# Optimization experiments

Hardware: AMD Instinct MI355X
Metric: run time of the kernel (lower is better)

The kernel has to match this reference:

```python
import jax, jax.numpy as jnp
import numpy as np

N = 50000   # nodes
E = 1000000 # edges
D_IN = 64
D_OUT = 64
R = 16      # relations (num_rels == num_bases)


def setup_inputs() -> dict:
    key = jax.random.key(0)
    k1, k2, k3, k4, k5, k6, k7 = jax.random.split(key, 7)
    node_features = jax.random.normal(k1, (N, D_IN), dtype=jnp.float32)
    edge_src = jax.random.randint(k2, (E,), 0, N, dtype=jnp.int32)
    edge_dst = jax.random.randint(k3, (E,), 0, N, dtype=jnp.int32)
    edge_type = jax.random.randint(k4, (E,), 0, R, dtype=jnp.int32)
    edge_norm = jax.random.uniform(k5, (E,), dtype=jnp.float32)
    weight = jax.random.normal(k6, (R, D_IN, D_OUT), dtype=jnp.float32) * 0.1
    bias = jax.random.normal(k7, (D_OUT,), dtype=jnp.float32) * 0.1
    return {
        "node_features": node_features,
        "edge_src": edge_src,
        "edge_dst": edge_dst,
        "edge_type": edge_type,
        "edge_norm": edge_norm,
        "weight": weight,
        "bias": bias,
    }


def reference(node_features, edge_src, edge_dst, edge_type, edge_norm, weight, bias):
    # gather source features and per-edge relation weight matrices
    h_src = node_features[edge_src]              # [E, D_IN]
    w = weight[edge_type]                        # [E, D_IN, D_OUT]
    # per-edge bmm: [E,1,D_IN] @ [E,D_IN,D_OUT] -> [E,D_OUT]
    msg = jnp.einsum('ed,edo->eo', h_src, w)
    msg = msg * edge_norm[:, None]               # norm scaling
    # scatter-sum aggregation over destination nodes
    node_repr = jax.ops.segment_sum(msg, edge_dst, num_segments=N)  # [N, D_OUT]
    node_repr = node_repr + bias
    return jax.nn.relu(node_repr)
```

## Files before the change

kernel.cpp:

```cpp
#include <hip/hip_runtime.h>
#include <hip/hip_bf16.h>


#define NN 50000
#define EE 1000000
#define RR 16
#define NBLK 256
#define EPB 3907
#define BSH 6
#define NBUK 782
#define NS (NBUK * NBLK)
#define SCAP 2048

typedef __attribute__((ext_vector_type(8))) short short8;
typedef __attribute__((ext_vector_type(4))) float f32x4;

static __device__ inline unsigned short f2bf(float f) {
  union { __hip_bfloat16 h; unsigned short u; } cv;
  cv.h = __float2bfloat16(f);
  return cv.u;
}
static __device__ inline float bf2f(unsigned short u) {
  union { unsigned i; float f; } cv;
  cv.i = ((unsigned)u) << 16;
  return cv.f;
}

__global__ __launch_bounds__(256) void k_wt(const float* __restrict__ W,
                                            unsigned short* __restrict__ Wt) {
  __shared__ __align__(16) unsigned short Wl[64][72];
  const int r = blockIdx.x, tid = threadIdx.x;
  for (int i = tid; i < 4096; i += 256) Wl[i & 63][i >> 6] = f2bf(W[(r << 12) + i]);
  __syncthreads();
  const int o = tid >> 2, kc = (tid & 3) << 4;
  const short8 v0 = *reinterpret_cast<const short8*>(&Wl[o][kc]);
  const short8 v1 = *reinterpret_cast<const short8*>(&Wl[o][kc + 8]);
  unsigned short* dst = Wt + (r << 12) + (o << 6) + kc;
  *reinterpret_cast<short8*>(dst) = v0;
  *reinterpret_cast<short8*>(dst + 8) = v1;
}

__global__ __launch_bounds__(256) void k_gemm_hist(const float* __restrict__ nf,
                                                   const unsigned short* __restrict__ Wt,
                                                   const int* __restrict__ edst,
                                                   unsigned short* __restrict__ X,
                                                   int* __restrict__ cntT) {
  __shared__ __align__(16) char smem[4 * 64 * 72 * 2];
  const int bid = blockIdx.x, tid = threadIdx.x;
  if (bid < NBLK) {
    int* cnt = reinterpret_cast<int*>(smem);
    for (int i = tid; i < NBUK; i += 256) cnt[i] = 0;
    __syncthreads();
    const int e0 = bid * EPB, e1 = min(EE, e0 + EPB);
    for (int e = e0 + tid; e < e1; e += 256) atomicAdd(&cnt[edst[e] >> BSH], 1);
    __syncthreads();
    for (int i = tid; i < NBUK; i += 256) cntT[i * NBLK + bid] = cnt[i];
    return;
  }
  auto Wl = reinterpret_cast<unsigned short(*)[64][72]>(smem);
  const int g = bid - NBLK;
  const int bx = g >> 2, r0 = (g & 3) << 2;
  const int lane = tid & 63, wv = tid >> 6;
  const int lr = lane & 15, lg = lane >> 4;
  const int node = (bx << 6) + (wv << 4) + lr;
  #pragma unroll
  for (int rr = 0; rr < 4; ++rr) {
    const unsigned short* src = Wt + (((size_t)(r0 + rr)) << 12) + (tid << 4);
    const short8 v0 = *reinterpret_cast<const short8*>(src);
    const short8 v1 = *reinterpret_cast<const short8*>(src + 8);
    unsigned short* dst = &Wl[rr][tid >> 2][(tid & 3) << 4];
    *reinterpret_cast<short8*>(dst) = v0;
    *reinterpret_cast<short8*>(dst + 8) = v1;
  }
  short8 bf0, bf1;
  if (node < NN) {
    const float* ap = nf + (size_t)node * 64 + lg * 8;
    float4 v0 = *reinterpret_cast<const float4*>(ap);
    float4 v1 = *reinterpret_cast<const float4*>(ap + 4);
    float4 v2 = *reinterpret_cast<const float4*>(ap + 32);
    float4 v3 = *reinterpret_cast<const float4*>(ap + 36);
    bf0 = short8{(short)f2bf(v0.x), (short)f2bf(v0.y), (short)f2bf(v0.z), (short)f2bf(v0.w),
                 (short)f2bf(v1.x), (short)f2bf(v1.y), (short)f2bf(v1.z), (short)f2bf(v1.w)};
    bf1 = short8{(short)f2bf(v2.x), (short)f2bf(v2.y), (short)f2bf(v2.z), (short)f2bf(v2.w),
                 (short)f2bf(v3.x), (short)f2bf(v3.y), (short)f2bf(v3.z), (short)f2bf(v3.w)};
  } else {
    bf0 = short8{0, 0, 0, 0, 0, 0, 0, 0};
    bf1 = bf0;
  }
  __syncthreads();
  #pragma unroll
  for (int rr = 0; rr < 4; ++rr) {
    const int r = r0 + rr;
    short8 a[8];
    #pragma unroll
    for (int c = 0; c < 4; ++c) {
      a[2 * c] = *reinterpret_cast<const short8*>(&Wl[rr][(c << 4) + lr][lg << 3]);
      a[2 * c + 1] = *reinterpret_cast<const short8*>(&Wl[rr][(c << 4) + lr][32 + (lg << 3)]);
    }
    f32x4 acc[4];
    #pragma unroll
    for (int c = 0; c < 4; ++c) {
      acc[c] = f32x4{0.f, 0.f, 0.f, 0.f};
      acc[c] = __builtin_amdgcn_mfma_f32_16x16x32_bf16(a[2 * c], bf0, acc[c], 0, 0, 0);
      acc[c] = __builtin_amdgcn_mfma_f32_16x16x32_bf16(a[2 * c + 1], bf1, acc[c], 0, 0, 0);
    }
    if (node < NN) {
      #pragma unroll
      for (int c = 0; c < 4; ++c) {
        uint2 p;
        p.x = (unsigned)f2bf(acc[c][0]) | ((unsigned)f2bf(acc[c][1]) << 16);
        p.y = (unsigned)f2bf(acc[c][2]) | ((unsigned)f2bf(acc[c][3]) << 16);
        *reinterpret_cast<uint2*>(&X[((size_t)r * NN + node) * 64 + (c << 4) + (lg << 2)]) = p;
      }
    }
  }
}

__global__ __launch_bounds__(256) void k_scan_a(const int* __restrict__ cntT,
                                                int* __restrict__ offsT,
                                                int* __restrict__ bsum) {
  __shared__ int s[256];
  const int t = threadIdx.x;
  const int i = blockIdx.x * 256 + t;
  const int v = cntT[i];
  s[t] = v;
  __syncthreads();
  #pragma unroll
  for (int off = 1; off < 256; off <<= 1) {
    const int x = (t >= off) ? s[t - off] : 0;
    __syncthreads();
    s[t] += x;
    __syncthreads();
  }
  offsT[i] = s[t] - v;
  if (t == 255) bsum[blockIdx.x] = s[255];
}

__global__ __launch_bounds__(1024) void k_scan_b(const int* __restrict__ bsum,
                                                 int* __restrict__ bsum2) {
  __shared__ int s[1024];
  const int t = threadIdx.x;
  const int v = (t < NBUK) ? bsum[t] : 0;
  s[t] = v;
  __syncthreads();
  #pragma unroll
  for (int off = 1; off < 1024; off <<= 1) {
    const int x = (t >= off) ? s[t - off] : 0;
    __syncthreads();
    s[t] += x;
    __syncthreads();
  }
  if (t < NBUK) bsum2[t] = s[t] - v;
  if (t == NBUK) bsum2[NBUK] = EE;
}

__global__ __launch_bounds__(256) void k_scatter(const int* __restrict__ esrc,
                                                 const int* __restrict__ edst,
                                                 const int* __restrict__ etyp,
                                                 const float* __restrict__ enorm,
                                                 const int* __restrict__ offsT,
                                                 const int* __restrict__ bsum2,
                                                 uint2* __restrict__ rec) {
  __shared__ int cur[NBUK];
  const int bl = blockIdx.x, tid = threadIdx.x;
  for (int i = tid; i < NBUK; i += 256) cur[i] = offsT[i * NBLK + bl] + bsum2[i];
  __syncthreads();
  const int e0 = bl * EPB, e1 = min(EE, e0 + EPB);
  for (int e = e0 + tid; e < e1; e += 256) {
    const int d = edst[e];
    const int pos = atomicAdd(&cur[d >> BSH], 1);
    rec[pos] = make_uint2(((unsigned)(etyp[e] * NN + esrc[e]) << 6) | (unsigned)(d & 63),
                          __float_as_uint(enorm[e]));
  }
}

__global__ __launch_bounds__(1024) void k_sortgather(const int* __restrict__ bsum2,
                                                     const uint2* __restrict__ rec,
                                                     const unsigned short* __restrict__ X,
                                                     const float* __restrict__ bias,
                                                     float* __restrict__ out) {
  __shared__ uint2 sbuf[SCAP];
  __shared__ uint2 sbuf2[SCAP];
  __shared__ int cnt[64], cur[64], nstart[65];
  const int bu = blockIdx.x, tid = threadIdx.x;
  const int s = bsum2[bu];
  const int e = bsum2[bu + 1];
  const int n = e - s;
  const int lane = tid & 63, wv = tid >> 6;
  const int quarter = lane >> 4, d4 = lane & 15;
  if (tid < 64) cnt[tid] = 0;
  __syncthreads();
  const bool sorted = (n <= SCAP);
  if (sorted) {
    for (int i = tid; i < n; i += 1024) {
      const uint2 r = rec[s + i];
      sbuf[i] = r;
      atomicAdd(&cnt[r.x & 63u], 1);
    }
    __syncthreads();
    if (tid < 64) {
      const int v = cnt[tid];
      int x = v;
      #pragma unroll
      for (int off = 1; off < 64; off <<= 1) {
        const int t = __shfl_up(x, off, 64);
        if (tid >= off) x += t;
      }
      cur[tid] = x - v;
      nstart[tid] = x - v;
      if (tid == 63) nstart[64] = n;
    }
    __syncthreads();
    for (int i = tid; i < n; i += 1024) {
      const uint2 r = sbuf[i];
      const int pos = atomicAdd(&cur[r.x & 63u], 1);
      sbuf2[pos] = r;
    }
    __syncthreads();
  }
  #pragma unroll
  for (int k = 0; k < 4; ++k) {
    const int nl = (wv << 2) + k;
    const int w = (bu << BSH) + nl;
    float4 acc = {0.f, 0.f, 0.f, 0.f};
    if (sorted) {
      const int jb = nstart[nl], je = nstart[nl + 1];
      for (int base = jb; base < je; base += 64) {
        const int deg = min(64, je - base);
        unsigned rxs = 0;
        float rns = 0.f;
        if (lane < deg) {
          const uint2 r = sbuf2[base + lane];
          rxs = r.x >> 6;
          rns = __uint_as_float(r.y);
        }
        int u = 0;
        for (; u + 16 <= deg; u += 16) {
          unsigned row[4];
          float nm[4];
          uint2 xv[4];
          #pragma unroll
          for (int q = 0; q < 4; ++q) {
            const int i = u + 4 * q + quarter;
            row[q] = (unsigned)__shfl((int)rxs, i, 64);
            nm[q] = __shfl(rns, i, 64);
          }
          #pragma unroll
          for (int q = 0; q < 4; ++q)
            xv[q] = *reinterpret_cast<const uint2*>(X + (size_t)row[q] * 64 + (d4 << 2));
          #pragma unroll
          for (int q = 0; q < 4; ++q) {
            acc.x = fmaf(nm[q], bf2f((unsigned short)(xv[q].x & 0xffffu)), acc.x);
            acc.y = fmaf(nm[q], bf2f((unsigned short)(xv[q].x >> 16)), acc.y);
            acc.z = fmaf(nm[q], bf2f((unsigned short)(xv[q].y & 0xffffu)), acc.z);
            acc.w = fmaf(nm[q], bf2f((unsigned short)(xv[q].y >> 16)), acc.w);
          }
        }
        for (; u + 8 <= deg; u += 8) {
          const int i0 = u + quarter, i1 = u + 4 + quarter;
          const unsigned row0 = (unsigned)__shfl((int)rxs, i0, 64);
          const float n0 = __shfl(rns, i0, 64);
          const unsigned row1 = (unsigned)__shfl((int)rxs, i1, 64);
          const float n1 = __shfl(rns, i1, 64);
          const uint2 x0 = *reinterpret_cast<const uint2*>(X + (size_t)row0 * 64 + (d4 << 2));
          const uint2 x1 = *reinterpret_cast<const uint2*>(X + (size_t)row1 * 64 + (d4 << 2));
          acc.x = fmaf(n0, bf2f((unsigned short)(x0.x & 0xffffu)), acc.x);
          acc.y = fmaf(n0, bf2f((unsigned short)(x0.x >> 16)), acc.y);
          acc.z = fmaf(n0, bf2f((unsigned short)(x0.y & 0xffffu)), acc.z);
          acc.w = fmaf(n0, bf2f((unsigned short)(x0.y >> 16)), acc.w);
          acc.x = fmaf(n1, bf2f((unsigned short)(x1.x & 0xffffu)), acc.x);
          acc.y = fmaf(n1, bf2f((unsigned short)(x1.x >> 16)), acc.y);
          acc.z = fmaf(n1, bf2f((unsigned short)(x1.y & 0xffffu)), acc.z);
          acc.w = fmaf(n1, bf2f((unsigned short)(x1.y >> 16)), acc.w);
        }
        for (; u < deg; u += 4) {
          const int i = u + quarter;
          const int ic = min(i, deg - 1);
          const unsigned row = (unsigned)__shfl((int)rxs, ic, 64);
          float nm = __shfl(rns, ic, 64);
          nm = (i < deg) ? nm : 0.f;
          const uint2 x = *reinterpret_cast<const uint2*>(X + (size_t)row * 64 + (d4 << 2));
          acc.x = fmaf(nm, bf2f((unsigned short)(x.x & 0xffffu)), acc.x);
          acc.y = fmaf(nm, bf2f((unsigned short)(x.x >> 16)), acc.y);
          acc.z = fmaf(nm, bf2f((unsigned short)(x.y & 0xffffu)), acc.z);
          acc.w = fmaf(nm, bf2f((unsigned short)(x.y >> 16)), acc.w);
        }
      }
    } else if (quarter == 0) {
      const unsigned dl = (unsigned)nl;
      for (int j = s; j < e; ++j) {
        const uint2 r = rec[j];
        if ((r.x & 63u) == dl) {
          const float nm = __uint_as_float(r.y);
          const uint2 x =
              *reinterpret_cast<const uint2*>(X + (size_t)(r.x >> 6) * 64 + (d4 << 2));
          acc.x = fmaf(nm, bf2f((unsigned short)(x.x & 0xffffu)), acc.x);
          acc.y = fmaf(nm, bf2f((unsigned short)(x.x >> 16)), acc.y);
          acc.z = fmaf(nm, bf2f((unsigned short)(x.y & 0xffffu)), acc.z);
          acc.w = fmaf(nm, bf2f((unsigned short)(x.y >> 16)), acc.w);
        }
      }
    }
    acc.x += __shfl_xor(acc.x, 16, 64);
    acc.y += __shfl_xor(acc.y, 16, 64);
    acc.z += __shfl_xor(acc.z, 16, 64);
    acc.w += __shfl_xor(acc.w, 16, 64);
    acc.x += __shfl_xor(acc.x, 32, 64);
    acc.y += __shfl_xor(acc.y, 32, 64);
    acc.z += __shfl_xor(acc.z, 32, 64);
    acc.w += __shfl_xor(acc.w, 32, 64);
    if (quarter == 0 && w < NN) {
      const float4 b = reinterpret_cast<const float4*>(bias)[d4];
      float4 o;
      o.x = fmaxf(acc.x + b.x, 0.f);
      o.y = fmaxf(acc.y + b.y, 0.f);
      o.z = fmaxf(acc.z + b.z, 0.f);
      o.w = fmaxf(acc.w + b.w, 0.f);
      reinterpret_cast<float4*>(out)[(size_t)w * 16 + d4] = o;
    }
  }
}

extern "C" void kernel_launch(void* const* d_in, const int* in_sizes, int n_in,
                              void* d_out, int out_size, void* d_ws, size_t ws_size,
                              hipStream_t stream) {
  const float* nf = (const float*)d_in[0];
  const int* esrc = (const int*)d_in[1];
  const int* edst = (const int*)d_in[2];
  const int* etyp = (const int*)d_in[3];
  const float* enorm = (const float*)d_in[4];
  const float* W = (const float*)d_in[5];
  const float* bias = (const float*)d_in[6];
  float* out = (float*)d_out;

  char* ws = (char*)d_ws;
  unsigned short* X = (unsigned short*)ws;
  unsigned short* Wt = (unsigned short*)(ws + 102400000);
  uint2* rec = (uint2*)(ws + 102531072);
  int* cntT = (int*)(ws + 110531072);
  int* offsT = (int*)(ws + 111331840);
  int* bsum = (int*)(ws + 112132608);
  int* bsum2 = (int*)(ws + 112135736);

  k_wt<<<RR, 256, 0, stream>>>(W, Wt);
  k_gemm_hist<<<NBLK + NBUK * 4, 256, 0, stream>>>(nf, Wt, edst, X, cntT);
  k_scan_a<<<NS / 256, 256, 0, stream>>>(cntT, offsT, bsum);
  k_scan_b<<<1, 1024, 0, stream>>>(bsum, bsum2);
  k_scatter<<<NBLK, 256, 0, stream>>>(esrc, edst, etyp, enorm, offsT, bsum2, rec);
  k_sortgather<<<NBUK, 1024, 0, stream>>>(bsum2, rec, X, bias, out);
}
```

Baseline: 95.45 us.

## Skip projected-feature writes for (node, relation) pairs no edge uses

New measurement: 140.5 us. 47.2% more time.

```diff
diff --git a/kernel.cpp b/kernel.cpp
--- a/kernel.cpp
+++ b/kernel.cpp
@@ -11,6 +11,7 @@
 #define NBUK 782
 #define NS (NBUK * NBLK)
 #define SCAP 2048
+#define NMW 25008
 
 typedef __attribute__((ext_vector_type(8))) short short8;
 typedef __attribute__((ext_vector_type(4))) float f32x4;
@@ -27,9 +28,11 @@
 }
 
 __global__ __launch_bounds__(256) void k_wt(const float* __restrict__ W,
-                                            unsigned short* __restrict__ Wt) {
+                                            unsigned short* __restrict__ Wt,
+                                            unsigned* __restrict__ mask) {
   __shared__ __align__(16) unsigned short Wl[64][72];
   const int r = blockIdx.x, tid = threadIdx.x;
+  for (int i = tid; i < NMW / RR; i += 256) mask[r * (NMW / RR) + i] = 0;
   for (int i = tid; i < 4096; i += 256) Wl[i & 63][i >> 6] = f2bf(W[(r << 12) + i]);
   __syncthreads();
   const int o = tid >> 2, kc = (tid & 3) << 4;
@@ -40,29 +43,35 @@
   *reinterpret_cast<short8*>(dst + 8) = v1;
 }
 
-__global__ __launch_bounds__(256) void k_gemm_hist(const float* __restrict__ nf,
-                                                   const unsigned short* __restrict__ Wt,
-                                                   const int* __restrict__ edst,
-                                                   unsigned short* __restrict__ X,
-                                                   int* __restrict__ cntT) {
-  __shared__ __align__(16) char smem[4 * 64 * 72 * 2];
-  const int bid = blockIdx.x, tid = threadIdx.x;
-  if (bid < NBLK) {
-    int* cnt = reinterpret_cast<int*>(smem);
-    for (int i = tid; i < NBUK; i += 256) cnt[i] = 0;
-    __syncthreads();
-    const int e0 = bid * EPB, e1 = min(EE, e0 + EPB);
-    for (int e = e0 + tid; e < e1; e += 256) atomicAdd(&cnt[edst[e] >> BSH], 1);
-    __syncthreads();
-    for (int i = tid; i < NBUK; i += 256) cntT[i * NBLK + bid] = cnt[i];
-    return;
-  }
-  auto Wl = reinterpret_cast<unsigned short(*)[64][72]>(smem);
-  const int g = bid - NBLK;
-  const int bx = g >> 2, r0 = (g & 3) << 2;
+__global__ __launch_bounds__(256) void k_hist(const int* __restrict__ esrc,
+                                              const int* __restrict__ edst,
+                                              const int* __restrict__ etyp,
+                                              int* __restrict__ cntT,
+                                              unsigned* __restrict__ mask) {
+  __shared__ int cnt[NBUK];
+  const int bl = blockIdx.x, tid = threadIdx.x;
+  for (int i = tid; i < NBUK; i += 256) cnt[i] = 0;
+  __syncthreads();
+  const int e0 = bl * EPB, e1 = min(EE, e0 + EPB);
+  for (int e = e0 + tid; e < e1; e += 256) {
+    atomicAdd(&cnt[edst[e] >> BSH], 1);
+    const unsigned bit = ((unsigned)esrc[e] << 4) | (unsigned)etyp[e];
+    atomicOr(&mask[bit >> 5], 1u << (bit & 31));
+  }
+  __syncthreads();
+  for (int i = tid; i < NBUK; i += 256) cntT[i * NBLK + bl] = cnt[i];
+}
+
+__global__ __launch_bounds__(256) void k_gemm(const float* __restrict__ nf,
+                                              const unsigned short* __restrict__ Wt,
+                                              const unsigned* __restrict__ mask,
+                                              unsigned short* __restrict__ X) {
+  __shared__ __align__(16) unsigned short Wl[4][64][72];
+  const int tid = threadIdx.x;
   const int lane = tid & 63, wv = tid >> 6;
   const int lr = lane & 15, lg = lane >> 4;
-  const int node = (bx << 6) + (wv << 4) + lr;
+  const int node = (blockIdx.x << 6) + (wv << 4) + lr;
+  const int r0 = blockIdx.y << 2;
   #pragma unroll
   for (int rr = 0; rr < 4; ++rr) {
     const unsigned short* src = Wt + (((size_t)(r0 + rr)) << 12) + (tid << 4);
@@ -73,7 +82,9 @@
     *reinterpret_cast<short8*>(dst + 8) = v1;
   }
   short8 bf0, bf1;
+  unsigned m16 = 0;
   if (node < NN) {
+    m16 = (mask[node >> 1] >> ((node & 1) << 4)) & 0xffffu;
     const float* ap = nf + (size_t)node * 64 + lg * 8;
     float4 v0 = *reinterpret_cast<const float4*>(ap);
     float4 v1 = *reinterpret_cast<const float4*>(ap + 4);
@@ -104,7 +115,7 @@
       acc[c] = __builtin_amdgcn_mfma_f32_16x16x32_bf16(a[2 * c], bf0, acc[c], 0, 0, 0);
       acc[c] = __builtin_amdgcn_mfma_f32_16x16x32_bf16(a[2 * c + 1], bf1, acc[c], 0, 0, 0);
     }
-    if (node < NN) {
+    if (node < NN && ((m16 >> r) & 1u)) {
       #pragma unroll
       for (int c = 0; c < 4; ++c) {
         uint2 p;
@@ -341,9 +352,12 @@
   int* offsT = (int*)(ws + 111331840);
   int* bsum = (int*)(ws + 112132608);
   int* bsum2 = (int*)(ws + 112135736);
-
-  k_wt<<<RR, 256, 0, stream>>>(W, Wt);
-  k_gemm_hist<<<NBLK + NBUK * 4, 256, 0, stream>>>(nf, Wt, edst, X, cntT);
+  unsigned* mask = (unsigned*)(ws + 112138868);
+
+  k_wt<<<RR, 256, 0, stream>>>(W, Wt, mask);
+  k_hist<<<NBLK, 256, 0, stream>>>(esrc, edst, etyp, cntT, mask);
+  dim3 g1(NBUK, 4);
+  k_gemm<<<g1, 256, 0, stream>>>(nf, Wt, mask, X);
   k_scan_a<<<NS / 256, 256, 0, stream>>>(cntT, offsT, bsum);
   k_scan_b<<<1, 1024, 0, stream>>>(bsum, bsum2);
   k_scatter<<<NBLK, 256, 0, stream>>>(esrc, edst, etyp, enorm, offsT, bsum2, rec);
```
